# Kernel optimization log

Hardware: AMD Instinct MI355X
Metric: run time of the kernel (lower is better)

## Reference

```python
import jax, jax.numpy as jnp
import numpy as np

HEADS = 8
DIM_HEAD = 64

def setup_inputs() -> dict:
    key = jax.random.key(0)
    ks = jax.random.split(key, 9)
    B, N1, N2, D = 4, 2048, 2048, 1024
    inner = HEADS * DIM_HEAD  # 512
    s_in = 1.0 / np.sqrt(D)
    s_inner = 1.0 / np.sqrt(inner)
    return {
        "x1": jax.random.normal(ks[0], (B, N1, D), jnp.float32),
        "x2": jax.random.normal(ks[1], (B, N2, D), jnp.float32),
        "Wq1": jax.random.normal(ks[2], (D, inner), jnp.float32) * s_in,
        "Wk1": jax.random.normal(ks[3], (D, inner), jnp.float32) * s_in,
        "Wv1": jax.random.normal(ks[4], (D, inner), jnp.float32) * s_in,
        "Wk2": jax.random.normal(ks[5], (D, inner), jnp.float32) * s_in,
        "Wv2": jax.random.normal(ks[6], (D, inner), jnp.float32) * s_in,
        "Wo": jax.random.normal(ks[7], (inner, D), jnp.float32) * s_inner,
        "bo": jnp.zeros((D,), jnp.float32),
    }

def reference(x1, x2, Wq1, Wk1, Wv1, Wk2, Wv2, Wo, bo):
    h, d = HEADS, DIM_HEAD
    scale = d ** (-0.5)
    B, N1, _ = x1.shape
    N2 = x2.shape[1]

    def split_heads(t, n):
        return t.reshape(B, n, h, d)  # [B, n, h, d]

    q1 = split_heads(x1 @ Wq1, N1)
    k1 = split_heads(x1 @ Wk1, N1)
    v1 = split_heads(x1 @ Wv1, N1)
    k2 = split_heads(x2 @ Wk2, N2)
    v2 = split_heads(x2 @ Wv2, N2)

    k = jnp.concatenate([k1, k2], axis=1)  # [B, N1+N2, h, d]
    v = jnp.concatenate([v1, v2], axis=1)

    # fp32 precision for QK^T (matches _ATTN_PRECISION == 'fp32')
    sim = jnp.einsum('bihd,bjhd->bhij', q1.astype(jnp.float32),
                     k.astype(jnp.float32)) * scale  # [B, h, N1, N1+N2]
    attn = jax.nn.softmax(sim, axis=-1)
    out = jnp.einsum('bhij,bjhd->bihd', attn, v)  # [B, N1, h, d]
    out = out.reshape(B, N1, h * d)
    return out @ Wo + bo
```

## Files before the change

kernel.cpp:

```cpp
#include <hip/hip_runtime.h>
#include <stdint.h>

typedef __bf16 bf16x8 __attribute__((ext_vector_type(8)));
typedef float f32x4 __attribute__((ext_vector_type(4)));
typedef unsigned short ushort_t;

#define MFMA16(a,b,c) __builtin_amdgcn_mfma_f32_16x16x32_bf16((a),(b),(c),0,0,0)

__device__ __forceinline__ unsigned short f2bf(float f){
    unsigned u = __builtin_bit_cast(unsigned, f);
    u += 0x7fffu + ((u>>16)&1u);
    return (unsigned short)(u>>16);
}
__device__ __forceinline__ unsigned pack2bf(float lo, float hi){
    unsigned a = __builtin_bit_cast(unsigned, lo) + 0x8000u;
    unsigned b = __builtin_bit_cast(unsigned, hi) + 0x8000u;
    return __builtin_amdgcn_perm(b, a, 0x07060302u);
}
__device__ __forceinline__ float fexp2(float x){
#if __has_builtin(__builtin_amdgcn_exp2f)
    return __builtin_amdgcn_exp2f(x);
#else
    return exp2f(x);
#endif
}

__device__ __forceinline__ void async16(ushort_t* lds, const ushort_t* g){
#if __has_builtin(__builtin_amdgcn_global_load_lds)
    __builtin_amdgcn_global_load_lds(
        (const __attribute__((address_space(1))) void*)g,
        (__attribute__((address_space(3))) void*)lds, 16, 0, 0);
#else
    const int l = (int)(threadIdx.x & 63u);
    *(uint4*)(lds + (size_t)l*8) = *(const uint4*)g;
#endif
}

__global__ __launch_bounds__(256) void convert_x(const float* __restrict__ src,
                                                 ushort_t* __restrict__ dst){
    size_t i = ((size_t)blockIdx.x*256 + threadIdx.x)*8;
    float4 a = *(const float4*)(src + i);
    float4 b = *(const float4*)(src + i + 4);
    uint4 o;
    o.x = pack2bf(a.x, a.y); o.y = pack2bf(a.z, a.w);
    o.z = pack2bf(b.x, b.y); o.w = pack2bf(b.z, b.w);
    *(uint4*)(dst + i) = o;
}

__global__ __launch_bounds__(256) void transpose_w(
    const float* __restrict__ w0, const float* __restrict__ w1,
    const float* __restrict__ w2, const float* __restrict__ w3,
    const float* __restrict__ w4,
    ushort_t* __restrict__ Wt1, ushort_t* __restrict__ Wt2)
{
    int z = blockIdx.z;
    const float* src; ushort_t* dst;
    if (z < 3)  { src = (z==0)?w0:((z==1)?w1:w2); dst = Wt1 + (size_t)z*512*1024; }
    else        { src = (z==3)?w3:w4;             dst = Wt2 + (size_t)(z-3)*512*1024; }
    const int K = 1024, N = 512;
    int k0 = blockIdx.x*32, n0 = blockIdx.y*32;
    __shared__ float T[32][33];
    int t = threadIdx.x;
    int kr = t>>3, nc = (t&7)*4;
    float4 v = *(const float4*)(src + (size_t)(k0+kr)*N + n0 + nc);
    T[kr][nc] = v.x; T[kr][nc+1] = v.y; T[kr][nc+2] = v.z; T[kr][nc+3] = v.w;
    __syncthreads();
    int nr = t>>3, kc = (t&7)*4;
    uint2 o;
    o.x = pack2bf(T[kc][nr],   T[kc+1][nr]);
    o.y = pack2bf(T[kc+2][nr], T[kc+3][nr]);
    *(uint2*)(dst + (size_t)(n0+nr)*K + k0 + kc) = o;
    (void)K;
}

__global__ __launch_bounds__(256) void transpose_wo(
    const float* __restrict__ src, ushort_t* __restrict__ dst)
{
    __shared__ float T[64][33];
    const int k0 = blockIdx.x*64;
    const int n0 = blockIdx.y*32;
    const int t = threadIdx.x;
    const int kr = t>>3, nc = (t&7)*4;
#pragma unroll
    for (int hf = 0; hf < 2; ++hf){
        float4 v = *(const float4*)(src + (size_t)(k0 + hf*32 + kr)*1024 + n0 + nc);
        T[hf*32+kr][nc]   = v.x; T[hf*32+kr][nc+1] = v.y;
        T[hf*32+kr][nc+2] = v.z; T[hf*32+kr][nc+3] = v.w;
    }
    __syncthreads();
    const int nr = t>>3, kc = (t&7)*8;
    ushort_t tmp[8];
#pragma unroll
    for (int e = 0; e < 8; ++e){
        int dp = kc + e;
        int d  = ((dp&3)<<4) | (dp>>2);
        tmp[e] = f2bf(T[d][nr]);
    }
    *(uint4*)(dst + (size_t)(n0+nr)*512 + k0 + kc) = *(uint4*)tmp;
}

template<int KD, int MODE>
__global__ __launch_bounds__(256) void gemm_bt(
    const ushort_t* __restrict__ A, const ushort_t* __restrict__ Bt,
    ushort_t* __restrict__ Qp, ushort_t* __restrict__ Kp, ushort_t* __restrict__ Vtp,
    float* __restrict__ outF, const float* __restrict__ bias, int koff)
{
    __shared__ ushort_t As[2][128][32];
    __shared__ ushort_t Bs[2][128][32];
    const int t = threadIdx.x;
    const int m0 = blockIdx.x*128, n0 = blockIdx.y*128;
    const int w = t>>6, l = t&63;
    const int quad = l>>4, lc = l&15;
    const int wr = (w>>1)*64, wc = (w&1)*64;

    f32x4 acc[4][4] = {};

    const int crow = l>>2;
    const int kseg = (l&3)*8;
    const ushort_t* gA0 = A  + (size_t)(m0 + w*32      + crow)*KD + kseg;
    const ushort_t* gA1 = A  + (size_t)(m0 + w*32 + 16 + crow)*KD + kseg;
    const ushort_t* gB0 = Bt + (size_t)(n0 + w*32      + crow)*KD + kseg;
    const ushort_t* gB1 = Bt + (size_t)(n0 + w*32 + 16 + crow)*KD + kseg;

    const int NK = KD/32;

    async16(&As[0][w*32][0],    gA0);
    async16(&As[0][w*32+16][0], gA1);
    async16(&Bs[0][w*32][0],    gB0);
    async16(&Bs[0][w*32+16][0], gB1);
    __syncthreads();

    for (int kk = 0; kk < NK; ++kk) {
        const int cur = kk & 1;
        if (kk + 1 < NK) {
            const int k0 = (kk+1)*32;
            const int nx = cur ^ 1;
            async16(&As[nx][w*32][0],    gA0 + k0);
            async16(&As[nx][w*32+16][0], gA1 + k0);
            async16(&Bs[nx][w*32][0],    gB0 + k0);
            async16(&Bs[nx][w*32+16][0], gB1 + k0);
        }
        bf16x8 af[4], bfv[4];
#pragma unroll
        for (int i = 0; i < 4; ++i) {
            af[i]  = *(const bf16x8*)&As[cur][wr + i*16 + lc][quad*8];
            bfv[i] = *(const bf16x8*)&Bs[cur][wc + i*16 + lc][quad*8];
        }
#pragma unroll
        for (int mt = 0; mt < 4; ++mt)
#pragma unroll
            for (int nt = 0; nt < 4; ++nt)
                acc[mt][nt] = MFMA16(af[mt], bfv[nt], acc[mt][nt]);
        __syncthreads();
    }

    if (MODE == 2) {
        float bv[4];
#pragma unroll
        for (int nt = 0; nt < 4; ++nt) bv[nt] = bias[n0 + wc + nt*16 + lc];
#pragma unroll
        for (int mt = 0; mt < 4; ++mt) {
            const int row = m0 + wr + mt*16 + quad*4;
#pragma unroll
            for (int nt = 0; nt < 4; ++nt) {
                const int col = n0 + wc + nt*16 + lc;
#pragma unroll
                for (int r = 0; r < 4; ++r)
                    outF[(size_t)(row+r)*1024 + col] = acc[mt][nt][r] + bv[nt];
            }
        }
    } else {
        const int sub = (MODE == 0) ? (n0>>9) : (1 + (n0>>9));
        const int hh  = ((n0 + wc)>>6) & 7;
        const int dp  = 4*lc;
        const float QSC = 0.18033688011112042f;
        if (sub == 0) {
#pragma unroll
            for (int mt = 0; mt < 4; ++mt) {
                const int row = m0 + wr + mt*16 + quad*4;
                const int b = row>>11, i = row & 2047;
#pragma unroll
                for (int r = 0; r < 4; ++r) {
                    uint2 o;
                    o.x = pack2bf(acc[mt][0][r]*QSC, acc[mt][1][r]*QSC);
                    o.y = pack2bf(acc[mt][2][r]*QSC, acc[mt][3][r]*QSC);
                    *(uint2*)(Qp + ((size_t)(b*8+hh)*2048 + i + r)*64 + dp) = o;
                }
            }
        } else if (sub == 1) {
#pragma unroll
            for (int mt = 0; mt < 4; ++mt) {
                const int row = m0 + wr + mt*16 + quad*4;
                const int b = row>>11, i = row & 2047;
#pragma unroll
                for (int r = 0; r < 4; ++r) {
                    uint2 o;
                    o.x = pack2bf(acc[mt][0][r], acc[mt][1][r]);
                    o.y = pack2bf(acc[mt][2][r], acc[mt][3][r]);
                    *(uint2*)(Kp + ((size_t)(b*8+hh)*4096 + koff + i + r)*64 + dp) = o;
                }
            }
        } else {
#pragma unroll
            for (int mt = 0; mt < 4; ++mt) {
                const int row = m0 + wr + mt*16 + quad*4;
                const int b = row>>11, i = row & 2047;
#pragma unroll
                for (int nt = 0; nt < 4; ++nt) {
                    uint2 o;
                    o.x = pack2bf(acc[mt][nt][0], acc[mt][nt][1]);
                    o.y = pack2bf(acc[mt][nt][2], acc[mt][nt][3]);
                    *(uint2*)(Vtp + ((size_t)(b*8+hh)*64 + dp + nt)*4096 + koff + i) = o;
                }
            }
        }
    }
}

__global__ __launch_bounds__(256) void flash_attn(
    const ushort_t* __restrict__ Q, const ushort_t* __restrict__ Kg,
    const ushort_t* __restrict__ Vt, ushort_t* __restrict__ AO)
{
    __shared__ ushort_t Ks[2][64][72];
    __shared__ ushort_t Vs[2][64][72];
    const int bh = blockIdx.x, qt = blockIdx.y;
    const int b = bh>>3, h = bh&7;
    const int t = threadIdx.x, wv = t>>6, l = t&63;
    const int quad = l>>4, lc = l&15;

    const ushort_t* qbase = Q + ((size_t)bh*2048 + qt*128 + wv*16 + lc)*64;
    bf16x8 qA0 = *(const bf16x8*)(qbase + quad*8);
    bf16x8 qA1 = *(const bf16x8*)(qbase + 32 + quad*8);
    bf16x8 qB0 = *(const bf16x8*)(qbase + 64*64 + quad*8);
    bf16x8 qB1 = *(const bf16x8*)(qbase + 64*64 + 32 + quad*8);

    const ushort_t* Kb = Kg + (size_t)bh*4096*64;
    const ushort_t* Vb = Vt + (size_t)bh*64*4096;

    const int srow   = t>>2;
    const int schunk = t&3;
    const ushort_t* kst = Kb + (size_t)srow*64   + schunk*16;
    const ushort_t* vst = Vb + (size_t)srow*4096 + schunk*16;
    const int vcol = (schunk>>1)*32 + (schunk&1)*4;

    float l0 = 0.0f, l1 = 0.0f;
    f32x4 o0[4] = {}, o1[4] = {};

    uint4 ka  = *(const uint4*)(kst);
    uint4 kb2 = *(const uint4*)(kst + 8);
    uint4 va  = *(const uint4*)(vst);
    uint4 vb2 = *(const uint4*)(vst + 8);

    for (int jt = 0; jt < 64; ++jt) {
        const int cur = jt & 1;
        ushort_t* ksd = &Ks[cur][srow][schunk*16];
        ushort_t* vsd = &Vs[cur][srow][vcol];
        *(uint4*)ksd     = ka;
        *(uint4*)(ksd+8) = kb2;
        { uint2 t0; t0.x = va.x;  t0.y = va.y;  *(uint2*)(vsd)      = t0; }
        { uint2 t1; t1.x = va.z;  t1.y = va.w;  *(uint2*)(vsd + 8)  = t1; }
        { uint2 t2; t2.x = vb2.x; t2.y = vb2.y; *(uint2*)(vsd + 16) = t2; }
        { uint2 t3; t3.x = vb2.z; t3.y = vb2.w; *(uint2*)(vsd + 24) = t3; }
        __syncthreads();
        if (jt < 63) {
            const int j0 = (jt+1)*64;
            ka  = *(const uint4*)(kst + (size_t)j0*64);
            kb2 = *(const uint4*)(kst + (size_t)j0*64 + 8);
            va  = *(const uint4*)(vst + j0);
            vb2 = *(const uint4*)(vst + j0 + 8);
        }

        f32x4 s0[4], s1[4];
#pragma unroll
        for (int kt = 0; kt < 4; ++kt) {
            bf16x8 kf0 = *(const bf16x8*)&Ks[cur][kt*16 + lc][quad*8];
            bf16x8 kf1 = *(const bf16x8*)&Ks[cur][kt*16 + lc][32 + quad*8];
            f32x4 z0 = {}, z1 = {};
            z0 = MFMA16(kf0, qA0, z0); z0 = MFMA16(kf1, qA1, z0);
            z1 = MFMA16(kf0, qB0, z1); z1 = MFMA16(kf1, qB1, z1);
            s0[kt] = z0; s1[kt] = z1;
        }

        union { unsigned u[8]; bf16x8 v[2]; } p0, p1;
        float rs0 = 0.0f, rs1 = 0.0f;
#pragma unroll
        for (int kt = 0; kt < 4; ++kt) {
            float a0 = fexp2(s0[kt][0]), a1v = fexp2(s0[kt][1]);
            float a2 = fexp2(s0[kt][2]), a3 = fexp2(s0[kt][3]);
            rs0 += (a0 + a1v) + (a2 + a3);
            p0.u[kt*2]   = pack2bf(a0, a1v);
            p0.u[kt*2+1] = pack2bf(a2, a3);
            float c0 = fexp2(s1[kt][0]), c1 = fexp2(s1[kt][1]);
            float c2 = fexp2(s1[kt][2]), c3 = fexp2(s1[kt][3]);
            rs1 += (c0 + c1) + (c2 + c3);
            p1.u[kt*2]   = pack2bf(c0, c1);
            p1.u[kt*2+1] = pack2bf(c2, c3);
        }
        l0 += rs0; l1 += rs1;

#pragma unroll
        for (int dt = 0; dt < 4; ++dt) {
            bf16x8 vf0 = *(const bf16x8*)&Vs[cur][dt*16 + lc][quad*8];
            bf16x8 vf1 = *(const bf16x8*)&Vs[cur][dt*16 + lc][32 + quad*8];
            o0[dt] = MFMA16(vf0, p0.v[0], o0[dt]);
            o0[dt] = MFMA16(vf1, p0.v[1], o0[dt]);
            o1[dt] = MFMA16(vf0, p1.v[0], o1[dt]);
            o1[dt] = MFMA16(vf1, p1.v[1], o1[dt]);
        }
    }

    l0 += __shfl_xor(l0, 16); l0 += __shfl_xor(l0, 32);
    l1 += __shfl_xor(l1, 16); l1 += __shfl_xor(l1, 32);
    float li0 = 1.0f / l0, li1 = 1.0f / l1;

    const int qA = qt*128 + wv*16 + lc;
    ushort_t* aodA = AO + ((size_t)b*2048 + qA)*512 + h*64 + quad*4;
    ushort_t* aodB = aodA + (size_t)64*512;
#pragma unroll
    for (int dt = 0; dt < 4; ++dt) {
        uint2 oa, ob;
        oa.x = pack2bf(o0[dt][0]*li0, o0[dt][1]*li0);
        oa.y = pack2bf(o0[dt][2]*li0, o0[dt][3]*li0);
        *(uint2*)(aodA + dt*16) = oa;
        ob.x = pack2bf(o1[dt][0]*li1, o1[dt][1]*li1);
        ob.y = pack2bf(o1[dt][2]*li1, o1[dt][3]*li1);
        *(uint2*)(aodB + dt*16) = ob;
    }
}

extern "C" void kernel_launch(void* const* d_in, const int* in_sizes, int n_in,
                              void* d_out, int out_size, void* d_ws, size_t ws_size,
                              hipStream_t stream)
{
    const float* x1  = (const float*)d_in[0];
    const float* x2  = (const float*)d_in[1];
    const float* Wq1 = (const float*)d_in[2];
    const float* Wk1 = (const float*)d_in[3];
    const float* Wv1 = (const float*)d_in[4];
    const float* Wk2 = (const float*)d_in[5];
    const float* Wv2 = (const float*)d_in[6];
    const float* Wo  = (const float*)d_in[7];
    const float* bo  = (const float*)d_in[8];
    float* out = (float*)d_out;

    ushort_t* ws  = (ushort_t*)d_ws;
    ushort_t* Xc1 = ws;
    ushort_t* Xc2 = Xc1 + 8388608;
    ushort_t* Wt1 = Xc2 + 8388608;
    ushort_t* Wt2 = Wt1 + 1572864;
    ushort_t* Wot = Wt2 + 1048576;
    ushort_t* Qp  = Wot + 524288;
    ushort_t* Kp  = Qp  + 4194304;
    ushort_t* Vtp = Kp  + 8388608;
    ushort_t* AOp = Xc2;

    convert_x<<<4096, 256, 0, stream>>>(x1, Xc1);
    convert_x<<<4096, 256, 0, stream>>>(x2, Xc2);
    transpose_w<<<dim3(32,16,5), 256, 0, stream>>>(Wq1,Wk1,Wv1,Wk2,Wv2, Wt1,Wt2);
    transpose_wo<<<dim3(8,32), 256, 0, stream>>>(Wo, Wot);

    gemm_bt<1024,0><<<dim3(64,12), 256, 0, stream>>>(Xc1, Wt1, Qp, Kp, Vtp, nullptr, nullptr, 0);
    gemm_bt<1024,1><<<dim3(64,8),  256, 0, stream>>>(Xc2, Wt2, Qp, Kp, Vtp, nullptr, nullptr, 2048);

    flash_attn<<<dim3(32,16), 256, 0, stream>>>(Qp, Kp, Vtp, AOp);

    gemm_bt<512,2><<<dim3(64,8), 256, 0, stream>>>(AOp, Wot, nullptr, nullptr, nullptr, out, bo, 0);
}
```

Baseline: 296.0 us.

## Tile V-transpose layout for contiguous loads and halve attention query tile

The V projection epilogue now writes V^T in 64-key tiles, with the bf16 elements pre-permuted into the column order the attention kernel's LDS staging expects. Each attention tile load therefore becomes one contiguous 16-element chunk per thread with plain 128-bit LDS stores. The attention kernel also processes 64 queries per block instead of 128, doubling the grid to 1024 blocks for better occupancy and load balance. The cost is that K/V tiles are reloaded twice as often per query, and each block gets half the MFMA work per LDS load.

Result: slower. 309.0 us (+4.4%).

```diff
diff --git a/kernel.cpp b/kernel.cpp
--- a/kernel.cpp
+++ b/kernel.cpp
@@ -57,7 +57,7 @@
     const float* src; ushort_t* dst;
     if (z < 3)  { src = (z==0)?w0:((z==1)?w1:w2); dst = Wt1 + (size_t)z*512*1024; }
     else        { src = (z==3)?w3:w4;             dst = Wt2 + (size_t)(z-3)*512*1024; }
-    const int K = 1024, N = 512;
+    const int N = 512;
     int k0 = blockIdx.x*32, n0 = blockIdx.y*32;
     __shared__ float T[32][33];
     int t = threadIdx.x;
@@ -69,8 +69,7 @@
     uint2 o;
     o.x = pack2bf(T[kc][nr],   T[kc+1][nr]);
     o.y = pack2bf(T[kc+2][nr], T[kc+3][nr]);
-    *(uint2*)(dst + (size_t)(n0+nr)*K + k0 + kc) = o;
-    (void)K;
+    *(uint2*)(dst + (size_t)(n0+nr)*1024 + k0 + kc) = o;
 }
 
 __global__ __launch_bounds__(256) void transpose_wo(
@@ -205,12 +204,14 @@
             for (int mt = 0; mt < 4; ++mt) {
                 const int row = m0 + wr + mt*16 + quad*4;
                 const int b = row>>11, i = row & 2047;
+                const int tile = (koff + i) >> 6;
+                const int slot = 32*(mt>>1) + 4*(mt&1) + 8*quad;
 #pragma unroll
                 for (int nt = 0; nt < 4; ++nt) {
                     uint2 o;
                     o.x = pack2bf(acc[mt][nt][0], acc[mt][nt][1]);
                     o.y = pack2bf(acc[mt][nt][2], acc[mt][nt][3]);
-                    *(uint2*)(Vtp + ((size_t)(b*8+hh)*64 + dp + nt)*4096 + koff + i) = o;
+                    *(uint2*)(Vtp + (((size_t)(b*8+hh)*64 + tile)*64 + dp + nt)*64 + slot) = o;
                 }
             }
         }
@@ -228,23 +229,19 @@
     const int t = threadIdx.x, wv = t>>6, l = t&63;
     const int quad = l>>4, lc = l&15;
 
-    const ushort_t* qbase = Q + ((size_t)bh*2048 + qt*128 + wv*16 + lc)*64;
-    bf16x8 qA0 = *(const bf16x8*)(qbase + quad*8);
-    bf16x8 qA1 = *(const bf16x8*)(qbase + 32 + quad*8);
-    bf16x8 qB0 = *(const bf16x8*)(qbase + 64*64 + quad*8);
-    bf16x8 qB1 = *(const bf16x8*)(qbase + 64*64 + 32 + quad*8);
+    const ushort_t* qbase = Q + ((size_t)bh*2048 + qt*64 + wv*16 + lc)*64;
+    bf16x8 qf0 = *(const bf16x8*)(qbase + quad*8);
+    bf16x8 qf1 = *(const bf16x8*)(qbase + 32 + quad*8);
 
     const ushort_t* Kb = Kg + (size_t)bh*4096*64;
     const ushort_t* Vb = Vt + (size_t)bh*64*4096;
 
-    const int srow   = t>>2;
-    const int schunk = t&3;
-    const ushort_t* kst = Kb + (size_t)srow*64   + schunk*16;
-    const ushort_t* vst = Vb + (size_t)srow*4096 + schunk*16;
-    const int vcol = (schunk>>1)*32 + (schunk&1)*4;
-
-    float l0 = 0.0f, l1 = 0.0f;
-    f32x4 o0[4] = {}, o1[4] = {};
+    const int srow = t>>2, sseg = (t&3)*16;
+    const ushort_t* kst = Kb + (size_t)t*16;
+    const ushort_t* vst = Vb + (size_t)t*16;
+
+    float l_i = 0.0f;
+    f32x4 oacc[4] = {};
 
     uint4 ka  = *(const uint4*)(kst);
     uint4 kb2 = *(const uint4*)(kst + 8);
@@ -253,78 +250,65 @@
 
     for (int jt = 0; jt < 64; ++jt) {
         const int cur = jt & 1;
-        ushort_t* ksd = &Ks[cur][srow][schunk*16];
-        ushort_t* vsd = &Vs[cur][srow][vcol];
+        ushort_t* ksd = &Ks[cur][srow][sseg];
+        ushort_t* vsd = &Vs[cur][srow][sseg];
         *(uint4*)ksd     = ka;
         *(uint4*)(ksd+8) = kb2;
-        { uint2 t0; t0.x = va.x;  t0.y = va.y;  *(uint2*)(vsd)      = t0; }
-        { uint2 t1; t1.x = va.z;  t1.y = va.w;  *(uint2*)(vsd + 8)  = t1; }
-        { uint2 t2; t2.x = vb2.x; t2.y = vb2.y; *(uint2*)(vsd + 16) = t2; }
-        { uint2 t3; t3.x = vb2.z; t3.y = vb2.w; *(uint2*)(vsd + 24) = t3; }
+        *(uint4*)vsd     = va;
+        *(uint4*)(vsd+8) = vb2;
         __syncthreads();
         if (jt < 63) {
-            const int j0 = (jt+1)*64;
-            ka  = *(const uint4*)(kst + (size_t)j0*64);
-            kb2 = *(const uint4*)(kst + (size_t)j0*64 + 8);
+            const size_t j0 = (size_t)(jt+1)*4096;
+            ka  = *(const uint4*)(kst + j0);
+            kb2 = *(const uint4*)(kst + j0 + 8);
             va  = *(const uint4*)(vst + j0);
             vb2 = *(const uint4*)(vst + j0 + 8);
         }
 
-        f32x4 s0[4], s1[4];
+        f32x4 st[4];
 #pragma unroll
         for (int kt = 0; kt < 4; ++kt) {
             bf16x8 kf0 = *(const bf16x8*)&Ks[cur][kt*16 + lc][quad*8];
             bf16x8 kf1 = *(const bf16x8*)&Ks[cur][kt*16 + lc][32 + quad*8];
-            f32x4 z0 = {}, z1 = {};
-            z0 = MFMA16(kf0, qA0, z0); z0 = MFMA16(kf1, qA1, z0);
-            z1 = MFMA16(kf0, qB0, z1); z1 = MFMA16(kf1, qB1, z1);
-            s0[kt] = z0; s1[kt] = z1;
-        }
-
-        union { unsigned u[8]; bf16x8 v[2]; } p0, p1;
-        float rs0 = 0.0f, rs1 = 0.0f;
+            f32x4 z = {};
+            z = MFMA16(kf0, qf0, z);
+            z = MFMA16(kf1, qf1, z);
+            st[kt] = z;
+        }
+
+        union { unsigned u[8]; bf16x8 v[2]; } pf;
+        float rs = 0.0f;
 #pragma unroll
         for (int kt = 0; kt < 4; ++kt) {
-            float a0 = fexp2(s0[kt][0]), a1v = fexp2(s0[kt][1]);
-            float a2 = fexp2(s0[kt][2]), a3 = fexp2(s0[kt][3]);
-            rs0 += (a0 + a1v) + (a2 + a3);
-            p0.u[kt*2]   = pack2bf(a0, a1v);
-            p0.u[kt*2+1] = pack2bf(a2, a3);
-            float c0 = fexp2(s1[kt][0]), c1 = fexp2(s1[kt][1]);
-            float c2 = fexp2(s1[kt][2]), c3 = fexp2(s1[kt][3]);
-            rs1 += (c0 + c1) + (c2 + c3);
-            p1.u[kt*2]   = pack2bf(c0, c1);
-            p1.u[kt*2+1] = pack2bf(c2, c3);
-        }
-        l0 += rs0; l1 += rs1;
+            float a0 = fexp2(st[kt][0]), a1 = fexp2(st[kt][1]);
+            float a2 = fexp2(st[kt][2]), a3 = fexp2(st[kt][3]);
+            rs += (a0 + a1) + (a2 + a3);
+            pf.u[kt*2]   = pack2bf(a0, a1);
+            pf.u[kt*2+1] = pack2bf(a2, a3);
+        }
+        l_i += rs;
 
 #pragma unroll
         for (int dt = 0; dt < 4; ++dt) {
             bf16x8 vf0 = *(const bf16x8*)&Vs[cur][dt*16 + lc][quad*8];
             bf16x8 vf1 = *(const bf16x8*)&Vs[cur][dt*16 + lc][32 + quad*8];
-            o0[dt] = MFMA16(vf0, p0.v[0], o0[dt]);
-            o0[dt] = MFMA16(vf1, p0.v[1], o0[dt]);
-            o1[dt] = MFMA16(vf0, p1.v[0], o1[dt]);
-            o1[dt] = MFMA16(vf1, p1.v[1], o1[dt]);
-        }
-    }
-
-    l0 += __shfl_xor(l0, 16); l0 += __shfl_xor(l0, 32);
-    l1 += __shfl_xor(l1, 16); l1 += __shfl_xor(l1, 32);
-    float li0 = 1.0f / l0, li1 = 1.0f / l1;
-
-    const int qA = qt*128 + wv*16 + lc;
-    ushort_t* aodA = AO + ((size_t)b*2048 + qA)*512 + h*64 + quad*4;
-    ushort_t* aodB = aodA + (size_t)64*512;
+            oacc[dt] = MFMA16(vf0, pf.v[0], oacc[dt]);
+            oacc[dt] = MFMA16(vf1, pf.v[1], oacc[dt]);
+        }
+    }
+
+    l_i += __shfl_xor(l_i, 16);
+    l_i += __shfl_xor(l_i, 32);
+    float linv = 1.0f / l_i;
+
+    const int qg = qt*64 + wv*16 + lc;
+    ushort_t* aod = AO + ((size_t)b*2048 + qg)*512 + h*64 + quad*4;
 #pragma unroll
     for (int dt = 0; dt < 4; ++dt) {
-        uint2 oa, ob;
-        oa.x = pack2bf(o0[dt][0]*li0, o0[dt][1]*li0);
-        oa.y = pack2bf(o0[dt][2]*li0, o0[dt][3]*li0);
-        *(uint2*)(aodA + dt*16) = oa;
-        ob.x = pack2bf(o1[dt][0]*li1, o1[dt][1]*li1);
-        ob.y = pack2bf(o1[dt][2]*li1, o1[dt][3]*li1);
-        *(uint2*)(aodB + dt*16) = ob;
+        uint2 o;
+        o.x = pack2bf(oacc[dt][0]*linv, oacc[dt][1]*linv);
+        o.y = pack2bf(oacc[dt][2]*linv, oacc[dt][3]*linv);
+        *(uint2*)(aod + dt*16) = o;
     }
 }
 
@@ -362,7 +346,7 @@
     gemm_bt<1024,0><<<dim3(64,12), 256, 0, stream>>>(Xc1, Wt1, Qp, Kp, Vtp, nullptr, nullptr, 0);
     gemm_bt<1024,1><<<dim3(64,8),  256, 0, stream>>>(Xc2, Wt2, Qp, Kp, Vtp, nullptr, nullptr, 2048);
 
-    flash_attn<<<dim3(32,16), 256, 0, stream>>>(Qp, Kp, Vtp, AOp);
+    flash_attn<<<dim3(32,32), 256, 0, stream>>>(Qp, Kp, Vtp, AOp);
 
     gemm_bt<512,2><<<dim3(64,8), 256, 0, stream>>>(AOp, Wot, nullptr, nullptr, nullptr, out, bo, 0);
 }
```

## Split attention over key halves, fuse projection GEMMs, retile V layout

Applied to the files above, without the earlier changes.

Flash attention is split along the key axis into two halves via a third grid dimension. Each half writes unnormalised fp32 partial outputs and row sums, and a new reduce kernel combines them, normalises, and converts to bf16. This doubles the number of attention blocks to improve occupancy on the GPU. The two projection GEMMs are merged into one launch. V is stored in a 64x64 tile-contiguous transposed layout so attention can load each tile with contiguous 16-byte loads and stores. In exchange there is extra fp32 partial-output traffic and one more kernel launch.

After: 297.8 us. No clear change (+0.6%).

```diff
diff --git a/kernel.cpp b/kernel.cpp
--- a/kernel.cpp
+++ b/kernel.cpp
@@ -57,7 +57,7 @@
     const float* src; ushort_t* dst;
     if (z < 3)  { src = (z==0)?w0:((z==1)?w1:w2); dst = Wt1 + (size_t)z*512*1024; }
     else        { src = (z==3)?w3:w4;             dst = Wt2 + (size_t)(z-3)*512*1024; }
-    const int K = 1024, N = 512;
+    const int N = 512;
     int k0 = blockIdx.x*32, n0 = blockIdx.y*32;
     __shared__ float T[32][33];
     int t = threadIdx.x;
@@ -69,8 +69,7 @@
     uint2 o;
     o.x = pack2bf(T[kc][nr],   T[kc+1][nr]);
     o.y = pack2bf(T[kc+2][nr], T[kc+3][nr]);
-    *(uint2*)(dst + (size_t)(n0+nr)*K + k0 + kc) = o;
-    (void)K;
+    *(uint2*)(dst + (size_t)(n0+nr)*1024 + k0 + kc) = o;
 }
 
 __global__ __launch_bounds__(256) void transpose_wo(
@@ -99,11 +98,114 @@
     *(uint4*)(dst + (size_t)(n0+nr)*512 + k0 + kc) = *(uint4*)tmp;
 }
 
-template<int KD, int MODE>
-__global__ __launch_bounds__(256) void gemm_bt(
+__global__ __launch_bounds__(256) void proj_fused(
+    const ushort_t* __restrict__ X1, const ushort_t* __restrict__ X2,
+    const ushort_t* __restrict__ W1, const ushort_t* __restrict__ W2,
+    ushort_t* __restrict__ Qp, ushort_t* __restrict__ Kp, ushort_t* __restrict__ Vtp)
+{
+    __shared__ ushort_t As[2][128][32];
+    __shared__ ushort_t Bs[2][128][32];
+    const int t = threadIdx.x;
+    const int m0 = blockIdx.x*128;
+    const int y  = blockIdx.y;
+    const ushort_t* A; const ushort_t* Bt; int n0, koff, sub;
+    if (y < 12) { A = X1; Bt = W1; n0 = y*128;      koff = 0;    sub = n0>>9; }
+    else        { A = X2; Bt = W2; n0 = (y-12)*128; koff = 2048; sub = 1 + (n0>>9); }
+
+    const int w = t>>6, l = t&63;
+    const int quad = l>>4, lc = l&15;
+    const int wr = (w>>1)*64, wc = (w&1)*64;
+    const int KD = 1024;
+
+    f32x4 acc[4][4] = {};
+
+    const int crow = l>>2;
+    const int kseg = (l&3)*8;
+    const ushort_t* gA0 = A  + (size_t)(m0 + w*32      + crow)*KD + kseg;
+    const ushort_t* gA1 = A  + (size_t)(m0 + w*32 + 16 + crow)*KD + kseg;
+    const ushort_t* gB0 = Bt + (size_t)(n0 + w*32      + crow)*KD + kseg;
+    const ushort_t* gB1 = Bt + (size_t)(n0 + w*32 + 16 + crow)*KD + kseg;
+
+    async16(&As[0][w*32][0],    gA0);
+    async16(&As[0][w*32+16][0], gA1);
+    async16(&Bs[0][w*32][0],    gB0);
+    async16(&Bs[0][w*32+16][0], gB1);
+    __syncthreads();
+
+    for (int kk = 0; kk < 32; ++kk) {
+        const int cur = kk & 1;
+        if (kk + 1 < 32) {
+            const int k0 = (kk+1)*32;
+            const int nx = cur ^ 1;
+            async16(&As[nx][w*32][0],    gA0 + k0);
+            async16(&As[nx][w*32+16][0], gA1 + k0);
+            async16(&Bs[nx][w*32][0],    gB0 + k0);
+            async16(&Bs[nx][w*32+16][0], gB1 + k0);
+        }
+        bf16x8 af[4], bfv[4];
+#pragma unroll
+        for (int i = 0; i < 4; ++i) {
+            af[i]  = *(const bf16x8*)&As[cur][wr + i*16 + lc][quad*8];
+            bfv[i] = *(const bf16x8*)&Bs[cur][wc + i*16 + lc][quad*8];
+        }
+#pragma unroll
+        for (int mt = 0; mt < 4; ++mt)
+#pragma unroll
+            for (int nt = 0; nt < 4; ++nt)
+                acc[mt][nt] = MFMA16(af[mt], bfv[nt], acc[mt][nt]);
+        __syncthreads();
+    }
+
+    const int hh = ((n0 + wc)>>6) & 7;
+    const int dp = 4*lc;
+    const float QSC = 0.18033688011112042f;
+    if (sub == 0) {
+#pragma unroll
+        for (int mt = 0; mt < 4; ++mt) {
+            const int row = m0 + wr + mt*16 + quad*4;
+            const int b = row>>11, i = row & 2047;
+#pragma unroll
+            for (int r = 0; r < 4; ++r) {
+                uint2 o;
+                o.x = pack2bf(acc[mt][0][r]*QSC, acc[mt][1][r]*QSC);
+                o.y = pack2bf(acc[mt][2][r]*QSC, acc[mt][3][r]*QSC);
+                *(uint2*)(Qp + ((size_t)(b*8+hh)*2048 + i + r)*64 + dp) = o;
+            }
+        }
+    } else if (sub == 1) {
+#pragma unroll
+        for (int mt = 0; mt < 4; ++mt) {
+            const int row = m0 + wr + mt*16 + quad*4;
+            const int b = row>>11, i = row & 2047;
+#pragma unroll
+            for (int r = 0; r < 4; ++r) {
+                uint2 o;
+                o.x = pack2bf(acc[mt][0][r], acc[mt][1][r]);
+                o.y = pack2bf(acc[mt][2][r], acc[mt][3][r]);
+                *(uint2*)(Kp + ((size_t)(b*8+hh)*4096 + koff + i + r)*64 + dp) = o;
+            }
+        }
+    } else {
+#pragma unroll
+        for (int mt = 0; mt < 4; ++mt) {
+            const int row = m0 + wr + mt*16 + quad*4;
+            const int b = row>>11, i = row & 2047;
+            const int tile = (koff + i) >> 6;
+            const int slot = 32*(mt>>1) + 4*(mt&1) + 8*quad;
+#pragma unroll
+            for (int nt = 0; nt < 4; ++nt) {
+                uint2 o;
+                o.x = pack2bf(acc[mt][nt][0], acc[mt][nt][1]);
+                o.y = pack2bf(acc[mt][nt][2], acc[mt][nt][3]);
+                *(uint2*)(Vtp + (((size_t)(b*8+hh)*64 + tile)*64 + dp + nt)*64 + slot) = o;
+            }
+        }
+    }
+}
+
+__global__ __launch_bounds__(256) void out_gemm(
     const ushort_t* __restrict__ A, const ushort_t* __restrict__ Bt,
-    ushort_t* __restrict__ Qp, ushort_t* __restrict__ Kp, ushort_t* __restrict__ Vtp,
-    float* __restrict__ outF, const float* __restrict__ bias, int koff)
+    float* __restrict__ outF, const float* __restrict__ bias)
 {
     __shared__ ushort_t As[2][128][32];
     __shared__ ushort_t Bs[2][128][32];
@@ -112,6 +214,7 @@
     const int w = t>>6, l = t&63;
     const int quad = l>>4, lc = l&15;
     const int wr = (w>>1)*64, wc = (w&1)*64;
+    const int KD = 512;
 
     f32x4 acc[4][4] = {};
 
@@ -122,17 +225,15 @@
     const ushort_t* gB0 = Bt + (size_t)(n0 + w*32      + crow)*KD + kseg;
     const ushort_t* gB1 = Bt + (size_t)(n0 + w*32 + 16 + crow)*KD + kseg;
 
-    const int NK = KD/32;
-
     async16(&As[0][w*32][0],    gA0);
     async16(&As[0][w*32+16][0], gA1);
     async16(&Bs[0][w*32][0],    gB0);
     async16(&Bs[0][w*32+16][0], gB1);
     __syncthreads();
 
-    for (int kk = 0; kk < NK; ++kk) {
+    for (int kk = 0; kk < 16; ++kk) {
         const int cur = kk & 1;
-        if (kk + 1 < NK) {
+        if (kk + 1 < 16) {
             const int k0 = (kk+1)*32;
             const int nx = cur ^ 1;
             async16(&As[nx][w*32][0],    gA0 + k0);
@@ -154,76 +255,30 @@
         __syncthreads();
     }
 
-    if (MODE == 2) {
-        float bv[4];
-#pragma unroll
-        for (int nt = 0; nt < 4; ++nt) bv[nt] = bias[n0 + wc + nt*16 + lc];
-#pragma unroll
-        for (int mt = 0; mt < 4; ++mt) {
-            const int row = m0 + wr + mt*16 + quad*4;
-#pragma unroll
-            for (int nt = 0; nt < 4; ++nt) {
-                const int col = n0 + wc + nt*16 + lc;
-#pragma unroll
-                for (int r = 0; r < 4; ++r)
-                    outF[(size_t)(row+r)*1024 + col] = acc[mt][nt][r] + bv[nt];
-            }
-        }
-    } else {
-        const int sub = (MODE == 0) ? (n0>>9) : (1 + (n0>>9));
-        const int hh  = ((n0 + wc)>>6) & 7;
-        const int dp  = 4*lc;
-        const float QSC = 0.18033688011112042f;
-        if (sub == 0) {
-#pragma unroll
-            for (int mt = 0; mt < 4; ++mt) {
-                const int row = m0 + wr + mt*16 + quad*4;
-                const int b = row>>11, i = row & 2047;
-#pragma unroll
-                for (int r = 0; r < 4; ++r) {
-                    uint2 o;
-                    o.x = pack2bf(acc[mt][0][r]*QSC, acc[mt][1][r]*QSC);
-                    o.y = pack2bf(acc[mt][2][r]*QSC, acc[mt][3][r]*QSC);
-                    *(uint2*)(Qp + ((size_t)(b*8+hh)*2048 + i + r)*64 + dp) = o;
-                }
-            }
-        } else if (sub == 1) {
-#pragma unroll
-            for (int mt = 0; mt < 4; ++mt) {
-                const int row = m0 + wr + mt*16 + quad*4;
-                const int b = row>>11, i = row & 2047;
-#pragma unroll
-                for (int r = 0; r < 4; ++r) {
-                    uint2 o;
-                    o.x = pack2bf(acc[mt][0][r], acc[mt][1][r]);
-                    o.y = pack2bf(acc[mt][2][r], acc[mt][3][r]);
-                    *(uint2*)(Kp + ((size_t)(b*8+hh)*4096 + koff + i + r)*64 + dp) = o;
-                }
-            }
-        } else {
-#pragma unroll
-            for (int mt = 0; mt < 4; ++mt) {
-                const int row = m0 + wr + mt*16 + quad*4;
-                const int b = row>>11, i = row & 2047;
-#pragma unroll
-                for (int nt = 0; nt < 4; ++nt) {
-                    uint2 o;
-                    o.x = pack2bf(acc[mt][nt][0], acc[mt][nt][1]);
-                    o.y = pack2bf(acc[mt][nt][2], acc[mt][nt][3]);
-                    *(uint2*)(Vtp + ((size_t)(b*8+hh)*64 + dp + nt)*4096 + koff + i) = o;
-                }
-            }
+    float bv[4];
+#pragma unroll
+    for (int nt = 0; nt < 4; ++nt) bv[nt] = bias[n0 + wc + nt*16 + lc];
+#pragma unroll
+    for (int mt = 0; mt < 4; ++mt) {
+        const int row = m0 + wr + mt*16 + quad*4;
+#pragma unroll
+        for (int nt = 0; nt < 4; ++nt) {
+            const int col = n0 + wc + nt*16 + lc;
+#pragma unroll
+            for (int r = 0; r < 4; ++r)
+                outF[(size_t)(row+r)*1024 + col] = acc[mt][nt][r] + bv[nt];
         }
     }
 }
 
 __global__ __launch_bounds__(256) void flash_attn(
     const ushort_t* __restrict__ Q, const ushort_t* __restrict__ Kg,
-    const ushort_t* __restrict__ Vt, ushort_t* __restrict__ AO)
+    const ushort_t* __restrict__ Vt,
+    float* __restrict__ O0, float* __restrict__ O1, float* __restrict__ Lp)
 {
     __shared__ ushort_t Ks[2][64][72];
     __shared__ ushort_t Vs[2][64][72];
-    const int bh = blockIdx.x, qt = blockIdx.y;
+    const int bh = blockIdx.x, qt = blockIdx.y, z = blockIdx.z;
     const int b = bh>>3, h = bh&7;
     const int t = threadIdx.x, wv = t>>6, l = t&63;
     const int quad = l>>4, lc = l&15;
@@ -234,14 +289,12 @@
     bf16x8 qB0 = *(const bf16x8*)(qbase + 64*64 + quad*8);
     bf16x8 qB1 = *(const bf16x8*)(qbase + 64*64 + 32 + quad*8);
 
-    const ushort_t* Kb = Kg + (size_t)bh*4096*64;
-    const ushort_t* Vb = Vt + (size_t)bh*64*4096;
-
-    const int srow   = t>>2;
-    const int schunk = t&3;
-    const ushort_t* kst = Kb + (size_t)srow*64   + schunk*16;
-    const ushort_t* vst = Vb + (size_t)srow*4096 + schunk*16;
-    const int vcol = (schunk>>1)*32 + (schunk&1)*4;
+    const ushort_t* Kb = Kg + ((size_t)bh*4096 + (size_t)z*2048)*64;
+    const ushort_t* Vb = Vt + ((size_t)bh*4096 + (size_t)z*2048)*64;
+
+    const int srow = t>>2, sseg = (t&3)*16;
+    const ushort_t* kst = Kb + (size_t)t*16;
+    const ushort_t* vst = Vb + (size_t)t*16;
 
     float l0 = 0.0f, l1 = 0.0f;
     f32x4 o0[4] = {}, o1[4] = {};
@@ -251,21 +304,19 @@
     uint4 va  = *(const uint4*)(vst);
     uint4 vb2 = *(const uint4*)(vst + 8);
 
-    for (int jt = 0; jt < 64; ++jt) {
+    for (int jt = 0; jt < 32; ++jt) {
         const int cur = jt & 1;
-        ushort_t* ksd = &Ks[cur][srow][schunk*16];
-        ushort_t* vsd = &Vs[cur][srow][vcol];
+        ushort_t* ksd = &Ks[cur][srow][sseg];
+        ushort_t* vsd = &Vs[cur][srow][sseg];
         *(uint4*)ksd     = ka;
         *(uint4*)(ksd+8) = kb2;
-        { uint2 t0; t0.x = va.x;  t0.y = va.y;  *(uint2*)(vsd)      = t0; }
-        { uint2 t1; t1.x = va.z;  t1.y = va.w;  *(uint2*)(vsd + 8)  = t1; }
-        { uint2 t2; t2.x = vb2.x; t2.y = vb2.y; *(uint2*)(vsd + 16) = t2; }
-        { uint2 t3; t3.x = vb2.z; t3.y = vb2.w; *(uint2*)(vsd + 24) = t3; }
+        *(uint4*)vsd     = va;
+        *(uint4*)(vsd+8) = vb2;
         __syncthreads();
-        if (jt < 63) {
-            const int j0 = (jt+1)*64;
-            ka  = *(const uint4*)(kst + (size_t)j0*64);
-            kb2 = *(const uint4*)(kst + (size_t)j0*64 + 8);
+        if (jt < 31) {
+            const size_t j0 = (size_t)(jt+1)*4096;
+            ka  = *(const uint4*)(kst + j0);
+            kb2 = *(const uint4*)(kst + j0 + 8);
             va  = *(const uint4*)(vst + j0);
             vb2 = *(const uint4*)(vst + j0 + 8);
         }
@@ -311,21 +362,39 @@
 
     l0 += __shfl_xor(l0, 16); l0 += __shfl_xor(l0, 32);
     l1 += __shfl_xor(l1, 16); l1 += __shfl_xor(l1, 32);
-    float li0 = 1.0f / l0, li1 = 1.0f / l1;
-
-    const int qA = qt*128 + wv*16 + lc;
-    ushort_t* aodA = AO + ((size_t)b*2048 + qA)*512 + h*64 + quad*4;
-    ushort_t* aodB = aodA + (size_t)64*512;
+
+    float* OP = z ? O1 : O0;
+    const int qgA = qt*128 + wv*16 + lc;
+    size_t baseA = ((size_t)b*2048 + qgA)*512 + h*64 + quad*4;
+    size_t baseB = baseA + (size_t)64*512;
 #pragma unroll
     for (int dt = 0; dt < 4; ++dt) {
-        uint2 oa, ob;
-        oa.x = pack2bf(o0[dt][0]*li0, o0[dt][1]*li0);
-        oa.y = pack2bf(o0[dt][2]*li0, o0[dt][3]*li0);
-        *(uint2*)(aodA + dt*16) = oa;
-        ob.x = pack2bf(o1[dt][0]*li1, o1[dt][1]*li1);
-        ob.y = pack2bf(o1[dt][2]*li1, o1[dt][3]*li1);
-        *(uint2*)(aodB + dt*16) = ob;
-    }
+        *(f32x4*)(OP + baseA + dt*16) = o0[dt];
+        *(f32x4*)(OP + baseB + dt*16) = o1[dt];
+    }
+    if (quad == 0) {
+        Lp[(size_t)z*65536 + bh*2048 + qgA]      = l0;
+        Lp[(size_t)z*65536 + bh*2048 + qgA + 64] = l1;
+    }
+}
+
+__global__ __launch_bounds__(256) void reduce_o(
+    const float* __restrict__ O0, const float* __restrict__ O1,
+    const float* __restrict__ Lp, ushort_t* __restrict__ AO)
+{
+    size_t i = ((size_t)blockIdx.x*256 + threadIdx.x)*4;
+    int row = (int)(i >> 9);
+    int col = (int)(i & 511);
+    int b = row >> 11, q = row & 2047, h = col >> 6;
+    size_t li = (size_t)(b*8 + h)*2048 + q;
+    float lsum = Lp[li] + Lp[65536 + li];
+    float linv = 1.0f / lsum;
+    float4 a = *(const float4*)(O0 + i);
+    float4 c = *(const float4*)(O1 + i);
+    uint2 o;
+    o.x = pack2bf((a.x + c.x)*linv, (a.y + c.y)*linv);
+    o.y = pack2bf((a.z + c.z)*linv, (a.w + c.w)*linv);
+    *(uint2*)(AO + i) = o;
 }
 
 extern "C" void kernel_launch(void* const* d_in, const int* in_sizes, int n_in,
@@ -352,17 +421,22 @@
     ushort_t* Qp  = Wot + 524288;
     ushort_t* Kp  = Qp  + 4194304;
     ushort_t* Vtp = Kp  + 8388608;
-    ushort_t* AOp = Xc2;
+
+    float* Opart0 = (float*)Xc1;
+    float* Opart1 = (float*)Xc2;
+    float* Lp     = (float*)Wt1;
+    ushort_t* AOp = Qp;
 
     convert_x<<<4096, 256, 0, stream>>>(x1, Xc1);
     convert_x<<<4096, 256, 0, stream>>>(x2, Xc2);
     transpose_w<<<dim3(32,16,5), 256, 0, stream>>>(Wq1,Wk1,Wv1,Wk2,Wv2, Wt1,Wt2);
     transpose_wo<<<dim3(8,32), 256, 0, stream>>>(Wo, Wot);
 
-    gemm_bt<1024,0><<<dim3(64,12), 256, 0, stream>>>(Xc1, Wt1, Qp, Kp, Vtp, nullptr, nullptr, 0);
-    gemm_bt<1024,1><<<dim3(64,8),  256, 0, stream>>>(Xc2, Wt2, Qp, Kp, Vtp, nullptr, nullptr, 2048);
-
-    flash_attn<<<dim3(32,16), 256, 0, stream>>>(Qp, Kp, Vtp, AOp);
-
-    gemm_bt<512,2><<<dim3(64,8), 256, 0, stream>>>(AOp, Wot, nullptr, nullptr, nullptr, out, bo, 0);
-}
+    proj_fused<<<dim3(64,20), 256, 0, stream>>>(Xc1, Xc2, Wt1, Wt2, Qp, Kp, Vtp);
+
+    flash_attn<<<dim3(32,16,2), 256, 0, stream>>>(Qp, Kp, Vtp, Opart0, Opart1, Lp);
+
+    reduce_o<<<4096, 256, 0, stream>>>(Opart0, Opart1, Lp, AOp);
+
+    out_gemm<<<dim3(64,8), 256, 0, stream>>>(AOp, Wot, out, bo);
+}
```
